# Optimization experiments

Measured on AMD Instinct MI355X. Metric: run time of the kernel, lower is better.

Reference implementation:

```python
import jax, jax.numpy as jnp
import numpy as np


def setup_inputs() -> dict:
    key = jax.random.key(0)
    kz, kh, k0 = jax.random.split(key, 3)
    B, C, D, H, W = 2, 96, 32, 32, 32
    z = jax.random.uniform(kz, (B, C, D, H, W), dtype=jnp.float32)  # gate in [0,1]
    h_tilde = jax.random.normal(kh, (B, C, D, H, W), dtype=jnp.float32)  # candidate state
    h0 = jax.random.uniform(k0, (1,), dtype=jnp.float32)  # scalar initial state
    return {"z": z, "h_tilde": h_tilde, "h0": h0}


def reference(z, h_tilde, h0):
    """GruDirection3d with d1=d2=d3=1 (forward_3, no flips).

    The three wavefront slice-updates in the torch code jointly implement
        out[d, y, x] = z[d, y, x] * h_tilde[d, y, x]
                       + (1 - z[d, y, x]) * out[d-1, y-1, x-1]
    with out == h0 whenever any index goes below 0 (the padded border).
    We realize it as t_num = min(D, H, W) full-volume shifted updates: after
    iteration k, all voxels with min(d, y, x) <= k-1 hold their final value,
    so after t_num iterations the result matches the torch wavefront DP exactly.
    """
    B, C, D, H, W = z.shape
    t_num = min(D, H, W)  # static shapes -> python int, jit-safe
    # padded state: index 0 along each spatial axis is the h0 border (never written)
    h_pad = jnp.full((B, C, D + 1, H + 1, W + 1), h0[0], dtype=z.dtype)

    one = jnp.asarray(1, dtype=z.dtype)

    def step(h_pad, _):
        prev = h_pad[:, :, :-1, :-1, :-1]  # out[d-1, y-1, x-1] (with border = h0)
        new = z * h_tilde + (one - z) * prev
        return h_pad.at[:, :, 1:, 1:, 1:].set(new), None

    h_pad, _ = jax.lax.scan(step, h_pad, None, length=t_num)
    return h_pad[:, :, 1:, 1:, 1:]
```

## Files before the change

kernel.cpp:

```cpp
#include <hip/hip_runtime.h>


#define DD 32
#define PF 12

__global__ __launch_bounds__(256) void gru3d_helix_pin(
    const float* __restrict__ z,
    const float* __restrict__ ht,
    const float* __restrict__ h0p,
    float* __restrict__ out)
{
    const int blk  = blockIdx.x;
    const int slab = blk >> 2;
    const int agrp = blk & 3;
    const int tid  = threadIdx.x;
    const int a    = (agrp << 3) + (tid >> 5);
    const int b    = tid & 31;

    const float h0 = h0p[0];

    const size_t base = (size_t)slab * (DD * 1024);
    const float* __restrict__ zb = z   + base;
    const float* __restrict__ tb = ht  + base;
    float*       __restrict__ ob = out + base;

    auto off = [&](int d) -> int {
        return (d << 10) | (((a + d) & 31) << 5) | ((b + d) & 31);
    };

    float zr[PF], tr[PF];
    #pragma unroll
    for (int p = 0; p < PF; ++p) {
        zr[p] = zb[off(p)];
        tr[p] = tb[off(p)];
    }
    __builtin_amdgcn_sched_barrier(0);

    float h = h0;

    #pragma unroll
    for (int d = 0; d < DD; ++d) {
        const int s = d % PF;

        const bool border = (((a + d) & 31) == 0) | (((b + d) & 31) == 0);
        const float pred  = border ? h0 : h;

        h = zr[s] * (tr[s] - pred) + pred;
        ob[off(d)] = h;

        if (d + PF < DD) {
            zr[s] = zb[off(d + PF)];
            tr[s] = tb[off(d + PF)];
        }
        __builtin_amdgcn_sched_barrier(0);
    }
}

extern "C" void kernel_launch(void* const* d_in, const int* in_sizes, int n_in,
                              void* d_out, int out_size, void* d_ws, size_t ws_size,
                              hipStream_t stream) {
    const float* z  = (const float*)d_in[0];
    const float* ht = (const float*)d_in[1];
    const float* h0 = (const float*)d_in[2];
    float* out      = (float*)d_out;

    const int BC = 2 * 96;
    gru3d_helix_pin<<<dim3(BC * 4), dim3(256), 0, stream>>>(z, ht, h0, out);
}
```

Measured before the change: 93.45 us.

## Vectorize GRU wavefront to float4 rows with lane shuffle for the diagonal shift

Each thread now owns a 4-wide strip of one row instead of a single diagonal helix. It loads z and h_tilde as float4 and gets the x-1 neighbour from the adjacent lane with __shfl_up, while the y border resets all four values to h0. Blocks shrink to 64 threads, so there are a quarter as many threads, and the prefetch depth drops from 12 to 8. The goal is fewer, wider memory instructions, at the cost of a cross-lane shuffle on every step's dependency chain, less thread-level parallelism and fewer bytes in flight for hiding memory latency.

```diff
diff --git a/kernel.cpp b/kernel.cpp
--- a/kernel.cpp
+++ b/kernel.cpp
@@ -2,9 +2,9 @@
 
 
 #define DD 32
-#define PF 12
+#define PF 8
 
-__global__ __launch_bounds__(256) void gru3d_helix_pin(
+__global__ __launch_bounds__(64) void gru3d_row4(
     const float* __restrict__ z,
     const float* __restrict__ ht,
     const float* __restrict__ h0p,
@@ -12,10 +12,11 @@
 {
     const int blk  = blockIdx.x;
     const int slab = blk >> 2;
-    const int agrp = blk & 3;
-    const int tid  = threadIdx.x;
-    const int a    = (agrp << 3) + (tid >> 5);
-    const int b    = tid & 31;
+    const int band = blk & 3;
+    const int lane = threadIdx.x;
+    const int r    = lane >> 3;
+    const int bg   = lane & 7;
+    const int a    = (band << 3) | r;
 
     const float h0 = h0p[0];
 
@@ -25,32 +26,41 @@
     float*       __restrict__ ob = out + base;
 
     auto off = [&](int d) -> int {
-        return (d << 10) | (((a + d) & 31) << 5) | ((b + d) & 31);
+        return (d << 10) | (((a + d) & 31) << 5) | (bg << 2);
     };
 
-    float zr[PF], tr[PF];
+    float4 zr[PF], tr[PF];
     #pragma unroll
     for (int p = 0; p < PF; ++p) {
-        zr[p] = zb[off(p)];
-        tr[p] = tb[off(p)];
+        zr[p] = *reinterpret_cast<const float4*>(zb + off(p));
+        tr[p] = *reinterpret_cast<const float4*>(tb + off(p));
     }
     __builtin_amdgcn_sched_barrier(0);
 
-    float h = h0;
+    float4 h = make_float4(h0, h0, h0, h0);
 
     #pragma unroll
     for (int d = 0; d < DD; ++d) {
         const int s = d % PF;
 
-        const bool border = (((a + d) & 31) == 0) | (((b + d) & 31) == 0);
-        const float pred  = border ? h0 : h;
+        const float up = __shfl_up(h.w, 1);
+        float p0 = (bg == 0) ? h0 : up;
+        float p1 = h.x, p2 = h.y, p3 = h.z;
+        if (((a + d) & 31) == 0) {
+            p0 = h0; p1 = h0; p2 = h0; p3 = h0;
+        }
 
-        h = zr[s] * (tr[s] - pred) + pred;
-        ob[off(d)] = h;
+        const float4 zv = zr[s], tv = tr[s];
+        h.x = fmaf(zv.x, tv.x - p0, p0);
+        h.y = fmaf(zv.y, tv.y - p1, p1);
+        h.z = fmaf(zv.z, tv.z - p2, p2);
+        h.w = fmaf(zv.w, tv.w - p3, p3);
+
+        *reinterpret_cast<float4*>(ob + off(d)) = h;
 
         if (d + PF < DD) {
-            zr[s] = zb[off(d + PF)];
-            tr[s] = tb[off(d + PF)];
+            zr[s] = *reinterpret_cast<const float4*>(zb + off(d + PF));
+            tr[s] = *reinterpret_cast<const float4*>(tb + off(d + PF));
         }
         __builtin_amdgcn_sched_barrier(0);
     }
@@ -65,5 +75,5 @@
     float* out      = (float*)d_out;
 
     const int BC = 2 * 96;
-    gru3d_helix_pin<<<dim3(BC * 4), dim3(256), 0, stream>>>(z, ht, h0, out);
+    gru3d_row4<<<dim3(BC * 4), dim3(64), 0, stream>>>(z, ht, h0, out);
 }
```

Result: slower. 98.33 us (+5.2%).
